# Kernel optimization log

Measured on AMD Instinct MI355X. Metric: run time of the kernel, lower is better.

The kernel has to match this reference:

```python
import jax, jax.numpy as jnp
import numpy as np

T_STEPS = 500
NHEAD = 4
L_TRANS = 2

def _pe(L, D):
    pos = np.arange(L)[:, None].astype(np.float32)
    i = np.arange(D // 2)[None, :].astype(np.float32)
    ang = pos / np.power(10000.0, 2.0 * i / D)
    pe = np.zeros((L, D), np.float32)
    pe[:, 0::2] = np.sin(ang)
    pe[:, 1::2] = np.cos(ang)
    return jnp.asarray(pe)

def _ln(x, g, b):
    m = x.mean(-1, keepdims=True)
    v = ((x - m) ** 2).mean(-1, keepdims=True)
    return (x - m) / jnp.sqrt(v + 1e-5) * g + b

def _gcn(A, X, W1, b1, W2, b2, W3, b3):
    h = jax.nn.relu((A @ X) @ W1 + b1)
    h = jax.nn.relu((A @ h) @ W2 + b2)
    return (A @ h) @ W3 + b3

def _mha(h, Wq, bq, Wk, bk, Wv, bv, Wo, bo):
    B, L, D = h.shape
    dh = D // NHEAD
    q = (h @ Wq + bq).reshape(B, L, NHEAD, dh)
    k = (h @ Wk + bk).reshape(B, L, NHEAD, dh)
    v = (h @ Wv + bv).reshape(B, L, NHEAD, dh)
    s = jnp.einsum('blhd,bmhd->bhlm', q, k) / jnp.sqrt(jnp.float32(dh))
    a = jax.nn.softmax(s, axis=-1)
    o = jnp.einsum('bhlm,bmhd->blhd', a, v).reshape(B, L, D)
    return o @ Wo + bo


def setup_inputs() -> dict:
    key = jax.random.key(0)
    ks = jax.random.split(key, 24)
    N_FP, N_WORD, DIM, HID = 10000, 4096, 20, 512
    HD1, HD2, LOUT, TDIM, FF = 128, 64, 3, 20, 2048
    N_ATOMS, N_RES, N_EDGES = 256, 4096, 65536
    w = lambda k, shp, s=0.05: jax.random.normal(k, shp, jnp.float32) * s
    idx_aa = jax.random.randint(ks[0], (N_RES,), 0, 20)
    x = jax.nn.one_hot(idx_aa, 20, dtype=jnp.float32)  # node one-hots
    adj_s = (jax.random.uniform(ks[1], (N_ATOMS, N_ATOMS)) < 0.1).astype(jnp.float32)
    return dict(
        x=x,
        smileadjacency=adj_s,
        emb_fp=w(ks[2], (N_FP, DIM)),
        emb_word=w(ks[3], (N_WORD, HID), 0.02),
        gW1=w(ks[4], (DIM, HD1)), gb1=jnp.zeros((HD1,), jnp.float32),
        gW2=w(ks[5], (HD1, HD2)), gb2=jnp.zeros((HD2,), jnp.float32),
        gW3=w(ks[6], (HD2, DIM)), gb3=jnp.zeros((DIM,), jnp.float32),
        Wq=w(ks[7], (L_TRANS, HID, HID)), bq=jnp.zeros((L_TRANS, HID), jnp.float32),
        Wk=w(ks[8], (L_TRANS, HID, HID)), bk=jnp.zeros((L_TRANS, HID), jnp.float32),
        Wv=w(ks[9], (L_TRANS, HID, HID)), bv=jnp.zeros((L_TRANS, HID), jnp.float32),
        Wo=w(ks[10], (L_TRANS, HID, HID)), bo=jnp.zeros((L_TRANS, HID), jnp.float32),
        ln1g=jnp.ones((L_TRANS, HID), jnp.float32), ln1b=jnp.zeros((L_TRANS, HID), jnp.float32),
        Wff1=w(ks[11], (L_TRANS, HID, FF)), bff1=jnp.zeros((L_TRANS, FF), jnp.float32),
        Wff2=w(ks[12], (L_TRANS, FF, HID)), bff2=jnp.zeros((L_TRANS, HID), jnp.float32),
        ln2g=jnp.ones((L_TRANS, HID), jnp.float32), ln2b=jnp.zeros((L_TRANS, HID), jnp.float32),
        Wproj=w(ks[13], (HID, DIM)), bproj=jnp.zeros((DIM,), jnp.float32),
        Wout=w(ks[14], (LOUT, 4 * DIM, 4 * DIM)), bout=jnp.zeros((LOUT, 4 * DIM), jnp.float32),
        Wtime=w(ks[15], (1, TDIM)), btime=jnp.zeros((TDIM,), jnp.float32),
        fingerprints=jax.random.randint(ks[16], (N_ATOMS,), 0, N_FP),
        words=jax.random.randint(ks[17], (N_RES,), 0, N_WORD),
        batch=jnp.zeros((N_RES,), jnp.int32),
        edge_index=jax.random.randint(ks[18], (2, N_EDGES), 0, N_RES),
        t=250,
        layer_output=3,
        dropout=0,
    )


def reference(x, smileadjacency, emb_fp, emb_word, gW1, gb1, gW2, gb2, gW3, gb3,
              Wq, bq, Wk, bk, Wv, bv, Wo, bo, ln1g, ln1b, Wff1, bff1, Wff2, bff2,
              ln2g, ln2b, Wproj, bproj, Wout, bout, Wtime, btime,
              fingerprints, words, batch, edge_index, t, layer_output, dropout):
    # --- diffusion noise (cosine alpha_bar, blosum-style transition, uniform mixing) ---
    t_float = float(t) / T_STEPS
    s = 0.008
    ab = np.cos((t_float + s) / (1 + s) * np.pi / 2) ** 2 / (np.cos(s / (1 + s) * np.pi / 2) ** 2)
    ab = jnp.float32(ab)
    Qtb = ab * jnp.eye(20, dtype=jnp.float32) + (1.0 - ab) / 20.0  # [20,20]
    prob = jnp.einsum('nij,nj->ni', Qtb[None][batch], x[:, :20])    # [n,20]
    X_t = jax.random.categorical(jax.random.key(42), jnp.log(prob + 1e-9))
    X = jax.nn.one_hot(X_t, 20, dtype=jnp.float32)
    time_emb = jnp.array([[t_float]], jnp.float32) @ Wtime + btime  # [1,20]
    # --- substrate GCN ---
    fp_vec = emb_fp[fingerprints]                                   # [n_atoms, dim]
    sub = _gcn(smileadjacency, fp_vec, gW1, gb1, gW2, gb2, gW3, gb3).mean(0, keepdims=True)
    # --- sequence transformer ---
    h = emb_word[words][None] + _pe(words.shape[0], emb_word.shape[1])[None]  # [1,L,hid]
    for l in range(L_TRANS):
        a = _mha(h, Wq[l], bq[l], Wk[l], bk[l], Wv[l], bv[l], Wo[l], bo[l])
        h = _ln(h + a, ln1g[l], ln1b[l])
        ff = jax.nn.relu(h @ Wff1[l] + bff1[l]) @ Wff2[l] + bff2[l]
        h = _ln(h + ff, ln2g[l], ln2b[l])
    seq = (h[0] @ Wproj + bproj).mean(0, keepdims=True)             # [1,dim]
    # --- protein graph: vectorized adjacency scatter (replaces per-edge python loop) ---
    n = X.shape[0]
    adj = jnp.zeros((n, n), jnp.float32).at[edge_index[0], edge_index[1]].set(1.0)
    prot = _gcn(adj, X, gW1, gb1, gW2, gb2, gW3, gb3).mean(0, keepdims=True)
    # --- fusion head (dropout=0 / eval mode) ---
    cat = jnp.concatenate([sub, prot, seq, time_emb], axis=1)        # [1, 4*dim]
    for j in range(int(layer_output)):
        cat = jax.nn.relu(cat) @ Wout[j] + bout[j]
    cat = jax.nn.relu(cat)
    return (cat, seq)
```

## Files before the change

### kernel.cpp

```cpp
#include <hip/hip_runtime.h>
#include <math.h>

typedef unsigned short ushort_t;
typedef __attribute__((ext_vector_type(8))) short bf16x8;
typedef __attribute__((ext_vector_type(4))) float f32x4;

__device__ inline float bf2f(unsigned u) { return __uint_as_float((u & 0xffffu) << 16); }
__device__ inline ushort_t f2bf(float f) {
    unsigned u = __float_as_uint(f);
    return (ushort_t)((u + 0x7fffu + ((u >> 16) & 1u)) >> 16);
}
__device__ inline void stv(float* p, float v) { *p = v; }
__device__ inline void stv(ushort_t* p, float v) { *p = f2bf(v); }
__device__ inline int guard_int(int raw, int lo, int hi) {
    if (raw >= lo && raw <= hi) return raw;
    float f = __int_as_float(raw);
    int v = (int)f;
    return (v >= lo && v <= hi) ? v : lo;
}

__device__ inline void tf2x32(unsigned k0, unsigned k1, unsigned x0, unsigned x1,
                              unsigned& o0, unsigned& o1) {
    unsigned ks2 = k0 ^ k1 ^ 0x1BD11BDAu;
    x0 += k0; x1 += k1;
#define TFR(r) { x0 += x1; x1 = (x1 << (r)) | (x1 >> (32 - (r))); x1 ^= x0; }
    TFR(13) TFR(15) TFR(26) TFR(6)  x0 += k1;  x1 += ks2 + 1u;
    TFR(17) TFR(29) TFR(16) TFR(24) x0 += ks2; x1 += k0 + 2u;
    TFR(13) TFR(15) TFR(26) TFR(6)  x0 += k0;  x1 += k1 + 3u;
    TFR(17) TFR(29) TFR(16) TFR(24) x0 += k1;  x1 += ks2 + 4u;
    TFR(13) TFR(15) TFR(26) TFR(6)  x0 += ks2; x1 += k0 + 5u;
#undef TFR
    o0 = x0; o1 = x1;
}

__global__ void k_sentinel(float* __restrict__ out, float val, int n) {
    int i = blockIdx.x * 128 + threadIdx.x;
    if (i < n) out[i] = val;
}

__global__ __launch_bounds__(256) void k_sample(const float* __restrict__ x,
                                                const int* __restrict__ t_ptr,
                                                float* __restrict__ X) {
    int i = blockIdx.x * 256 + threadIdx.x;
    if (i >= 4096) return;
    int tval = guard_int(t_ptr[0], 0, 500);
    double tf = (double)tval / 500.0;
    const double sc = 0.008;
    const double PI_HALF = 1.5707963267948966;
    double num = cos((tf + sc) / (1.0 + sc) * PI_HALF);
    double den = cos(sc / (1.0 + sc) * PI_HALF);
    float ab = (float)((num * num) / (den * den));
    float phi = (1.0f - ab) / 20.0f;
    float xv[20]; float sx = 0.f;
    for (int j = 0; j < 20; ++j) { xv[j] = x[i * 20 + j]; sx += xv[j]; }
    float best = -1e30f; int bj = 0;
    for (int j = 0; j < 20; ++j) {
        float prob = fmaxf(ab * xv[j] + phi * sx, 0.0f);
        float lp = logf(prob + 1e-9f);
        unsigned m = (unsigned)(i * 20 + j);
        unsigned o0, o1;
        tf2x32(0u, 42u, 0u, m, o0, o1);
        unsigned bits = o0 ^ o1;
        float u = __uint_as_float((bits >> 9) | 0x3f800000u) - 1.0f;
        if (u < 1.1754943508222875e-38f) u = 1.1754943508222875e-38f;
        float gmb = -logf(-logf(u));
        float z = lp + gmb;
        if (z > best) { best = z; bj = j; }
    }
    for (int j = 0; j < 20; ++j) X[i * 20 + j] = (j == bj) ? 1.0f : 0.0f;
}

__global__ __launch_bounds__(256) void k_gather_fp(const float* __restrict__ emb,
                                                   const int* __restrict__ idx,
                                                   float* __restrict__ out) {
    int i = blockIdx.x * 256 + threadIdx.x;
    if (i >= 256 * 20) return;
    int a = i / 20, d = i % 20;
    out[i] = emb[(size_t)idx[a] * 20 + d];
}

__global__ __launch_bounds__(256) void k_scatter_bits(const int* __restrict__ ei,
                                                      unsigned* __restrict__ bits) {
    int e = blockIdx.x * 256 + threadIdx.x;
    if (e >= 65536) return;
    int r = ei[e], c = ei[65536 + e];
    atomicOr(&bits[(size_t)r * 128 + (c >> 5)], 1u << (c & 31));
}

__global__ __launch_bounds__(256) void k_degree(const unsigned* __restrict__ BITS,
                                                float* __restrict__ deg) {
    int i = blockIdx.x * 256 + threadIdx.x;
    if (i >= 4096 * 128) return;
    unsigned bits = BITS[i];
    int base = (i & 127) * 32;
    while (bits) { int b = __ffs(bits) - 1; bits &= bits - 1; atomicAdd(&deg[base + b], 1.0f); }
}

__global__ __launch_bounds__(256) void k_embed(const float* __restrict__ embw,
                                               const int* __restrict__ words,
                                               float* __restrict__ H,
                                               ushort_t* __restrict__ Hb) {
    int idx = blockIdx.x * 256 + threadIdx.x;
    if (idx >= 4096 * 512) return;
    int pos = idx >> 9, d = idx & 511;
    float e = embw[(size_t)words[pos] * 512 + d];
    float expo = (float)(d >> 1) * (1.0f / 256.0f);
    float ang = (float)pos * exp2f(-expo * 13.287712379549449f);
    float pe = (d & 1) ? cosf(ang) : sinf(ang);
    float v = e + pe;
    H[idx] = v; Hb[idx] = f2bf(v);
}

__global__ __launch_bounds__(256) void k_colmean(const float* __restrict__ M, int R, int C,
                                                 float* __restrict__ out) {
    __shared__ float red[256];
    int c = blockIdx.x, t = threadIdx.x;
    float s = 0.f;
    for (int r = t; r < R; r += 256) s += M[(size_t)r * C + c];
    red[t] = s; __syncthreads();
    for (int o = 128; o; o >>= 1) { if (t < o) red[t] += red[t + o]; __syncthreads(); }
    if (t == 0) out[c] = red[0] / (float)R;
}

__global__ __launch_bounds__(256) void k_wcolsum(const float* __restrict__ M, int R, int C,
                                                 const float* __restrict__ w,
                                                 float* __restrict__ out) {
    __shared__ float red[256];
    int c = blockIdx.x, t = threadIdx.x;
    float s = 0.f;
    for (int r = t; r < R; r += 256) s += w[r] * M[(size_t)r * C + c];
    red[t] = s; __syncthreads();
    for (int o = 128; o; o >>= 1) { if (t < o) red[t] += red[t + o]; __syncthreads(); }
    if (t == 0) out[c] = red[0];
}

__global__ __launch_bounds__(256) void k_matvec20(int D, float scale,
                                                  const float* __restrict__ vec,
                                                  const float* __restrict__ W,
                                                  const float* __restrict__ bias,
                                                  float* __restrict__ out) {
    __shared__ float red[256];
    int c = blockIdx.x, t = threadIdx.x;
    float s = 0.f;
    for (int d = t; d < D; d += 256) s += vec[d] * W[(size_t)d * 20 + c];
    red[t] = s; __syncthreads();
    for (int o = 128; o; o >>= 1) { if (t < o) red[t] += red[t + o]; __syncthreads(); }
    if (t == 0) out[c] = red[0] * scale + bias[c];
}

__global__ void k_gather3(const float* __restrict__ a, const float* __restrict__ b,
                          const float* __restrict__ c, float* __restrict__ out) {
    int i = blockIdx.x * 256 + threadIdx.x;
    if (i >= 1536) return;
    out[i] = (i < 512) ? a[i] : (i < 1024) ? b[i - 512] : c[i - 1024];
}

__global__ __launch_bounds__(256) void k_castT(const float* __restrict__ in,
                                               ushort_t* __restrict__ out,
                                               int Kd, int Nd) {
    __shared__ float t[32][33];
    int bx = blockIdx.x * 32, by = blockIdx.y * 32;
    int tx = threadIdx.x & 31, ty = threadIdx.x >> 5;
#pragma unroll
    for (int i = 0; i < 4; ++i)
        t[ty + i * 8][tx] = in[(size_t)(by + ty + i * 8) * Nd + bx + tx];
    __syncthreads();
#pragma unroll
    for (int i = 0; i < 4; ++i)
        out[(size_t)(bx + ty + i * 8) * Kd + by + tx] = f2bf(t[tx][ty + i * 8]);
}

__global__ __launch_bounds__(256) void k_castT4(const float* __restrict__ in0,
                                                const float* __restrict__ in1,
                                                const float* __restrict__ in2,
                                                const float* __restrict__ in3,
                                                ushort_t* __restrict__ out) {
    __shared__ float t[32][33];
    int z = blockIdx.z;
    const float* in = (z == 0) ? in0 : (z == 1) ? in1 : (z == 2) ? in2 : in3;
    ushort_t* o = out + (size_t)z * 262144;
    int bx = blockIdx.x * 32, by = blockIdx.y * 32;
    int tx = threadIdx.x & 31, ty = threadIdx.x >> 5;
#pragma unroll
    for (int i = 0; i < 4; ++i)
        t[ty + i * 8][tx] = in[(size_t)(by + ty + i * 8) * 512 + bx + tx];
    __syncthreads();
#pragma unroll
    for (int i = 0; i < 4; ++i)
        o[(size_t)(bx + ty + i * 8) * 512 + by + tx] = f2bf(t[tx][ty + i * 8]);
}

__global__ __launch_bounds__(256) void k_transposeV(const ushort_t* __restrict__ in, int ldin,
                                                    ushort_t* __restrict__ out) {
    __shared__ ushort_t t[32][33];
    int bx = blockIdx.x * 32;
    int by = blockIdx.y * 32;
    int tx = threadIdx.x & 31, ty = threadIdx.x >> 5;
#pragma unroll
    for (int i = 0; i < 4; ++i)
        t[ty + i * 8][tx] = in[(size_t)(by + ty + i * 8) * ldin + bx + tx];
    __syncthreads();
#pragma unroll
    for (int i = 0; i < 4; ++i)
        out[(size_t)(bx + ty + i * 8) * 4096 + by + tx] = t[tx][ty + i * 8];
}

template<int BN, bool RELU, typename TC>
__global__ __launch_bounds__(256) void k_gemm_mfma2(int M, int N, int K, int lda,
        const ushort_t* __restrict__ A,
        const ushort_t* __restrict__ Bt,
        TC* __restrict__ C, int ldc,
        const float* __restrict__ bias) {
    constexpr int NJ = BN / 32;
    __shared__ ushort_t As[128][40];
    __shared__ ushort_t Bs[BN][40];
    int tid = threadIdx.x;
    int lane = tid & 63, wave = tid >> 6;
    int wr = wave >> 1, wc = wave & 1;
    int lrow = lane & 15, lq = lane >> 4;
    int br = blockIdx.y * 128, bc = blockIdx.x * BN;
    f32x4 acc[4][NJ];
#pragma unroll
    for (int i = 0; i < 4; ++i)
#pragma unroll
        for (int j = 0; j < NJ; ++j) { acc[i][j][0] = 0.f; acc[i][j][1] = 0.f; acc[i][j][2] = 0.f; acc[i][j][3] = 0.f; }
    int sr = tid >> 2, sseg = tid & 3;
    for (int k0 = 0; k0 < K; k0 += 32) {
#pragma unroll
        for (int it = 0; it < 2; ++it)
            *(uint4*)&As[sr + it * 64][sseg * 8] = *(const uint4*)&A[(size_t)(br + sr + it * 64) * lda + k0 + sseg * 8];
#pragma unroll
        for (int it = 0; it < BN / 64; ++it)
            *(uint4*)&Bs[sr + it * 64][sseg * 8] = *(const uint4*)&Bt[(size_t)(bc + sr + it * 64) * K + k0 + sseg * 8];
        __syncthreads();
        bf16x8 af[4], bfr[NJ];
#pragma unroll
        for (int i = 0; i < 4; ++i) af[i] = *(const bf16x8*)&As[wr * 64 + i * 16 + lrow][lq * 8];
#pragma unroll
        for (int j = 0; j < NJ; ++j) bfr[j] = *(const bf16x8*)&Bs[wc * (BN / 2) + j * 16 + lrow][lq * 8];
#pragma unroll
        for (int i = 0; i < 4; ++i)
#pragma unroll
            for (int j = 0; j < NJ; ++j)
                acc[i][j] = __builtin_amdgcn_mfma_f32_16x16x32_bf16(af[i], bfr[j], acc[i][j], 0, 0, 0);
        __syncthreads();
    }
#pragma unroll
    for (int i = 0; i < 4; ++i)
#pragma unroll
        for (int j = 0; j < NJ; ++j) {
            int col = bc + wc * (BN / 2) + j * 16 + lrow;
            float bv = bias ? bias[col] : 0.f;
#pragma unroll
            for (int r = 0; r < 4; ++r) {
                int row = br + wr * 64 + i * 16 + lq * 4 + r;
                float v = acc[i][j][r] + bv;
                if (RELU) v = fmaxf(v, 0.f);
                stv(&C[(size_t)row * ldc + col], v);
            }
        }
}

template<bool RELU>
__global__ __launch_bounds__(256) void k_gemm_nn(int M, int N, int K,
        const float* __restrict__ A, int lda,
        const float* __restrict__ B, int ldb,
        float* __restrict__ C, int ldc,
        const float* __restrict__ bias) {
    __shared__ float As[16][65];
    __shared__ float Bs[16][65];
    int tid = threadIdx.x;
    int tx = tid & 15, ty = tid >> 4;
    int br = blockIdx.y * 64, bc = blockIdx.x * 64;
    float acc[4][4] = {};
    for (int k0 = 0; k0 < K; k0 += 16) {
#pragma unroll
        for (int c0 = 0; c0 < 4; ++c0) {
            int r = (tid >> 4) + c0 * 16, kk = tid & 15;
            int gr = br + r, gk = k0 + kk;
            As[kk][r] = (gr < M && gk < K) ? A[(size_t)gr * lda + gk] : 0.f;
        }
#pragma unroll
        for (int c0 = 0; c0 < 4; ++c0) {
            int col = tid & 63, kk = (tid >> 6) + c0 * 4;
            int gc = bc + col, gk = k0 + kk;
            Bs[kk][col] = (gc < N && gk < K) ? B[(size_t)gk * ldb + gc] : 0.f;
        }
        __syncthreads();
#pragma unroll
        for (int kk = 0; kk < 16; ++kk) {
            float av[4], bv[4];
#pragma unroll
            for (int i2 = 0; i2 < 4; ++i2) av[i2] = As[kk][ty + 16 * i2];
#pragma unroll
            for (int j2 = 0; j2 < 4; ++j2) bv[j2] = Bs[kk][tx + 16 * j2];
#pragma unroll
            for (int i2 = 0; i2 < 4; ++i2)
#pragma unroll
                for (int j2 = 0; j2 < 4; ++j2) acc[i2][j2] += av[i2] * bv[j2];
        }
        __syncthreads();
    }
#pragma unroll
    for (int i2 = 0; i2 < 4; ++i2)
#pragma unroll
        for (int j2 = 0; j2 < 4; ++j2) {
            int r = br + ty + 16 * i2, c = bc + tx + 16 * j2;
            if (r < M && c < N) {
                float v = acc[i2][j2];
                if (bias) v += bias[c];
                if (RELU) v = fmaxf(v, 0.f);
                C[(size_t)r * ldc + c] = v;
            }
        }
}

template<int NC, int CH>
__global__ __launch_bounds__(256) void k_spmm_wave(
        const unsigned* __restrict__ BITS,
        const float* __restrict__ B, int ldb,
        float* __restrict__ C, int ldc) {
    int gw = blockIdx.x * 4 + (threadIdx.x >> 6);
    int lane = threadIdx.x & 63;
    int row = gw / CH, cb = (gw % CH) * NC;
    if (row >= 4096) return;
    float acc[NC];
#pragma unroll
    for (int j = 0; j < NC; ++j) acc[j] = 0.f;
    const unsigned* bw = &BITS[(size_t)row * 128];
#pragma unroll
    for (int i = 0; i < 2; ++i) {
        int wd = lane * 2 + i;
        unsigned bits = bw[wd];
        int base = wd * 32;
        while (bits) {
            int b = __ffs(bits) - 1; bits &= bits - 1;
            const float* br = &B[(size_t)(base + b) * ldb + cb];
#pragma unroll
            for (int j = 0; j < NC; ++j) acc[j] += br[j];
        }
    }
#pragma unroll
    for (int j = 0; j < NC; ++j) {
#pragma unroll
        for (int off = 1; off < 64; off <<= 1) acc[j] += __shfl_xor(acc[j], off, 64);
    }
    if (lane == 0)
#pragma unroll
        for (int j = 0; j < NC; ++j) C[(size_t)row * ldc + cb + j] = acc[j];
}

__global__ __launch_bounds__(256) void k_flash(const ushort_t* __restrict__ Qg, int ldq,
                                               const ushort_t* __restrict__ Kg, int ldk,
                                               const ushort_t* __restrict__ VTg,
                                               ushort_t* __restrict__ OP0,
                                               ushort_t* __restrict__ OP12,
                                               float* __restrict__ Mp,
                                               float* __restrict__ Lp) {
    __shared__ ushort_t Ks[32][136];
    __shared__ ushort_t Vt[128][40];
    __shared__ ushort_t Ps[4][16][40];
    __shared__ float    as_[4][16];
    __shared__ float    ls_[4][16];
    const int tid = threadIdx.x;
    const int lane = tid & 63, wid = tid >> 6;
    const int lrow = lane & 15, lq = lane >> 4;
    const int qb = blockIdx.x * 64, hh = blockIdx.y, z = blockIdx.z;
    const int kt0 = z * 43, kt1 = (z == 2) ? 128 : kt0 + 43;
    const float scale = 0.08838834764831845f;
    bf16x8 qf[4];
    {
        const ushort_t* qrow = &Qg[(size_t)(qb + wid * 16 + lrow) * ldq + hh * 128 + lq * 8];
#pragma unroll
        for (int s = 0; s < 4; ++s) qf[s] = *(const bf16x8*)&qrow[s * 32];
    }
    f32x4 o[8];
#pragma unroll
    for (int ct = 0; ct < 8; ++ct) { o[ct][0] = 0.f; o[ct][1] = 0.f; o[ct][2] = 0.f; o[ct][3] = 0.f; }
    float m = -INFINITY, l = 0.f;
    for (int kt = kt0; kt < kt1; ++kt) {
#pragma unroll
        for (int i = 0; i < 2; ++i) {
            int sid = tid + i * 256;
            int r = sid >> 4, sg = sid & 15;
            *(uint4*)&Ks[r][sg * 8] = *(const uint4*)&Kg[(size_t)(kt * 32 + r) * ldk + hh * 128 + sg * 8];
            int d = sid >> 2, c8 = sid & 3;
            *(uint4*)&Vt[d][c8 * 8] = *(const uint4*)&VTg[(size_t)(hh * 128 + d) * 4096 + kt * 32 + c8 * 8];
        }
        __syncthreads();
        f32x4 sa[2];
#pragma unroll
        for (int c = 0; c < 2; ++c) { sa[c][0] = 0.f; sa[c][1] = 0.f; sa[c][2] = 0.f; sa[c][3] = 0.f; }
#pragma unroll
        for (int c = 0; c < 2; ++c)
#pragma unroll
            for (int st = 0; st < 4; ++st) {
                bf16x8 kf = *(const bf16x8*)&Ks[c * 16 + lrow][st * 32 + lq * 8];
                sa[c] = __builtin_amdgcn_mfma_f32_16x16x32_bf16(kf, qf[st], sa[c], 0, 0, 0);
            }
        float s[8];
        float tm = -INFINITY;
#pragma unroll
        for (int c = 0; c < 2; ++c)
#pragma unroll
            for (int r = 0; r < 4; ++r) { float v = sa[c][r] * scale; s[c * 4 + r] = v; tm = fmaxf(tm, v); }
        tm = fmaxf(tm, __shfl_xor(tm, 16));
        tm = fmaxf(tm, __shfl_xor(tm, 32));
        bool up = tm > m;
        float mn = up ? tm : m;
        float a = up ? __expf(m - mn) : 1.0f;
        float su = 0.f;
        float p[8];
#pragma unroll
        for (int i = 0; i < 8; ++i) { p[i] = __expf(s[i] - mn); su += p[i]; }
        su += __shfl_xor(su, 16);
        su += __shfl_xor(su, 32);
        m = mn; l = l * a + su;
#pragma unroll
        for (int c = 0; c < 2; ++c)
#pragma unroll
            for (int r = 0; r < 4; ++r)
                Ps[wid][lrow][c * 16 + lq * 4 + r] = f2bf(p[c * 4 + r]);
        if (__any(up)) {
            if (lq == 0) as_[wid][lrow] = a;
            __builtin_amdgcn_s_waitcnt(0);
            float av[4];
#pragma unroll
            for (int r = 0; r < 4; ++r) av[r] = as_[wid][lq * 4 + r];
#pragma unroll
            for (int ct = 0; ct < 8; ++ct)
#pragma unroll
                for (int r = 0; r < 4; ++r) o[ct][r] *= av[r];
        } else {
            __builtin_amdgcn_s_waitcnt(0);
        }
        bf16x8 pf = *(const bf16x8*)&Ps[wid][lrow][lq * 8];
#pragma unroll
        for (int ct = 0; ct < 8; ++ct) {
            bf16x8 vf = *(const bf16x8*)&Vt[ct * 16 + lrow][lq * 8];
            o[ct] = __builtin_amdgcn_mfma_f32_16x16x32_bf16(pf, vf, o[ct], 0, 0, 0);
        }
        __syncthreads();
    }
    if (lq == 0) {
        Mp[(size_t)(z * 4 + hh) * 4096 + qb + wid * 16 + lrow] = m;
        Lp[(size_t)(z * 4 + hh) * 4096 + qb + wid * 16 + lrow] = l;
    }
    ushort_t* ob = (z == 0) ? OP0 : OP12 + (size_t)(z - 1) * 2097152;
#pragma unroll
    for (int ct = 0; ct < 8; ++ct)
#pragma unroll
        for (int r = 0; r < 4; ++r)
            ob[(size_t)(qb + wid * 16 + lq * 4 + r) * 512 + hh * 128 + ct * 16 + lrow] = f2bf(o[ct][r]);
}

__global__ __launch_bounds__(256) void k_fcomb(ushort_t* __restrict__ OP0,
                                               const ushort_t* __restrict__ OP12,
                                               const float* __restrict__ Mp,
                                               const float* __restrict__ Lp) {
    int idx = blockIdx.x * 256 + threadIdx.x;
    if (idx >= 4096 * 512) return;
    int row = idx >> 9, col = idx & 511;
    int hh = col >> 7;
    float m0 = Mp[hh * 4096 + row], m1 = Mp[(4 + hh) * 4096 + row], m2 = Mp[(8 + hh) * 4096 + row];
    float l0 = Lp[hh * 4096 + row], l1 = Lp[(4 + hh) * 4096 + row], l2 = Lp[(8 + hh) * 4096 + row];
    float mm = fmaxf(m0, fmaxf(m1, m2));
    float w0 = __expf(m0 - mm), w1 = __expf(m1 - mm), w2 = __expf(m2 - mm);
    float denom = l0 * w0 + l1 * w1 + l2 * w2;
    float o0 = bf2f(OP0[idx]), o1 = bf2f(OP12[idx]), o2 = bf2f(OP12[2097152 + idx]);
    OP0[idx] = f2bf((o0 * w0 + o1 * w1 + o2 * w2) / denom);
}

__global__ __launch_bounds__(256) void k_add_ln(const float* __restrict__ A,
                                                const float* __restrict__ B,
                                                float* __restrict__ O,
                                                ushort_t* __restrict__ Ob,
                                                const float* __restrict__ g,
                                                const float* __restrict__ b) {
    __shared__ float xr[512];
    __shared__ float red[256];
    int row = blockIdx.x, t = threadIdx.x;
    const float* a = A + (size_t)row * 512;
    const float* bb = B + (size_t)row * 512;
    float ls = 0.f;
    for (int j = t; j < 512; j += 256) { float v = a[j] + bb[j]; xr[j] = v; ls += v; }
    red[t] = ls; __syncthreads();
    for (int o = 128; o; o >>= 1) { if (t < o) red[t] += red[t + o]; __syncthreads(); }
    float mean = red[0] / 512.0f; __syncthreads();
    float lv = 0.f;
    for (int j = t; j < 512; j += 256) { float d = xr[j] - mean; lv += d * d; }
    red[t] = lv; __syncthreads();
    for (int o = 128; o; o >>= 1) { if (t < o) red[t] += red[t + o]; __syncthreads(); }
    float inv = 1.0f / sqrtf(red[0] / 512.0f + 1e-5f);
    float* o_ = O + (size_t)row * 512;
    ushort_t* ob = Ob + (size_t)row * 512;
    for (int j = t; j < 512; j += 256) {
        float v = (xr[j] - mean) * inv * g[j] + b[j];
        o_[j] = v; ob[j] = f2bf(v);
    }
}

__global__ __launch_bounds__(128) void k_fusion(const float* __restrict__ subv,
                                                const float* __restrict__ protv,
                                                const float* __restrict__ seqv,
                                                const float* __restrict__ Wtime,
                                                const float* __restrict__ btime,
                                                const float* __restrict__ Wout,
                                                const float* __restrict__ bout,
                                                const int* __restrict__ t_ptr,
                                                const int* __restrict__ lo_ptr,
                                                float* __restrict__ out) {
    __shared__ float cat[80];
    int t = threadIdx.x;
    int tval = guard_int(t_ptr[0], 0, 500);
    int L    = guard_int(lo_ptr[0], 0, 3);
    float tf = (float)((double)tval / 500.0);
    if (t < 20) {
        cat[t] = subv[t];
        cat[20 + t] = protv[t];
        cat[40 + t] = seqv[t];
        cat[60 + t] = tf * Wtime[t] + btime[t];
    }
    __syncthreads();
    for (int j = 0; j < L; ++j) {
        float acc = 0.f;
        if (t < 80) {
            for (int i2 = 0; i2 < 80; ++i2)
                acc += fmaxf(cat[i2], 0.f) * Wout[(size_t)j * 6400 + i2 * 80 + t];
            acc += bout[j * 80 + t];
        }
        __syncthreads();
        if (t < 80) cat[t] = acc;
        __syncthreads();
    }
    if (t < 80) out[t] = fmaxf(cat[t], 0.f);
    if (t < 20) out[80 + t] = seqv[t];
}

extern "C" void kernel_launch(void* const* d_in, const int* in_sizes, int n_in,
                              void* d_out, int out_size, void* d_ws, size_t ws_size,
                              hipStream_t stream) {
    static const int EXP[39] = {
        81920, 65536, 200000, 2097152, 2560, 128, 8192, 64, 1280, 20,
        524288, 1024, 524288, 1024, 524288, 1024, 524288, 1024, 1024, 1024,
        2097152, 4096, 2097152, 1024, 1024, 1024, 10240, 20, 19200, 240,
        20, 20, 256, 4096, 4096, 131072, 1, 1, 1 };
    float code = 0.f;
    if (n_in != 39) code = 900.f;
    else {
        for (int i = 0; i < 39; ++i)
            if (in_sizes[i] != EXP[i]) { code = 500.f + 4.f * (float)i; break; }
    }
    const size_t REQ = (size_t)46 * 1024 * 1024;
    if (code == 0.f && ws_size < REQ) code = (float)(ws_size >> 20);
    float* out = (float*)d_out;
    if (code != 0.f) {
        k_sentinel<<<1, 128, 0, stream>>>(out, -code, out_size);
        return;
    }

    const float* x_in   = (const float*)d_in[0];
    const float* adjs_in= (const float*)d_in[1];
    const float* embfp  = (const float*)d_in[2];
    const float* embw   = (const float*)d_in[3];
    const float* gW1 = (const float*)d_in[4];  const float* gb1 = (const float*)d_in[5];
    const float* gW2 = (const float*)d_in[6];  const float* gb2 = (const float*)d_in[7];
    const float* gW3 = (const float*)d_in[8];  const float* gb3 = (const float*)d_in[9];
    const float* Wq  = (const float*)d_in[10]; const float* bq  = (const float*)d_in[11];
    const float* Wk  = (const float*)d_in[12]; const float* bk  = (const float*)d_in[13];
    const float* Wv  = (const float*)d_in[14]; const float* bv  = (const float*)d_in[15];
    const float* Wo  = (const float*)d_in[16]; const float* bo  = (const float*)d_in[17];
    const float* ln1g= (const float*)d_in[18]; const float* ln1b= (const float*)d_in[19];
    const float* Wff1= (const float*)d_in[20]; const float* bff1= (const float*)d_in[21];
    const float* Wff2= (const float*)d_in[22]; const float* bff2= (const float*)d_in[23];
    const float* ln2g= (const float*)d_in[24]; const float* ln2b= (const float*)d_in[25];
    const float* Wproj=(const float*)d_in[26]; const float* bproj=(const float*)d_in[27];
    const float* Woutw=(const float*)d_in[28]; const float* boutw=(const float*)d_in[29];
    const float* Wtime=(const float*)d_in[30]; const float* btime=(const float*)d_in[31];
    const int* fingerprints = (const int*)d_in[32];
    const int* words        = (const int*)d_in[33];
    const int* edge_index   = (const int*)d_in[35];
    const int* t_ptr        = (const int*)d_in[36];
    const int* lo_ptr       = (const int*)d_in[37];

    char* wsb = (char*)d_ws;
    float*    misc = (float*)wsb;
    float*    H    = (float*)(wsb + ((size_t)2  << 20));
    ushort_t* Hb   = (ushort_t*)(wsb + ((size_t)10 << 20));
    ushort_t* QKVb = (ushort_t*)(wsb + ((size_t)14 << 20));
    ushort_t* Ob   = (ushort_t*)(wsb + ((size_t)26 << 20));
    ushort_t* FFHb = (ushort_t*)(wsb + ((size_t)14 << 20));
    float*    T    = (float*)(wsb + ((size_t)30 << 20));
    ushort_t* OP12 = (ushort_t*)(wsb + ((size_t)30 << 20));
    ushort_t* Wscr = (ushort_t*)(wsb + ((size_t)38 << 20));
    ushort_t* VTg  = (ushort_t*)(wsb + ((size_t)42 << 20));
    unsigned* ADJB = (unsigned*)(wsb + ((size_t)26 << 20));
    float* pt0  = (float*)(wsb + ((size_t)14 << 20));
    float* ph1  = pt0 + 81920;
    float* pt1  = ph1 + 524288;
    float* ph2  = pt1 + 524288;
    float* Xoh  = misc;
    float* fpv  = misc + 81920;
    float* st0  = misc + 87040;
    float* sh1  = misc + 92160;
    float* st1  = misc + 124928;
    float* sh2  = misc + 157696;
    float* st2  = misc + 174080;
    float* sgo  = misc + 190464;
    float* subv = misc + 277504;
    float* protv= misc + 277536;
    float* seqv = misc + 277568;
    float* hmean= misc + 280000;
    float* wsum = misc + 281000;
    float* deg  = misc + 282000;
    float* bqkv = misc + 287000;
    float* Mp   = misc + 300000;
    float* Lp   = misc + 360000;

    auto g2 = [](int M, int N) { return dim3((unsigned)((N + 63) / 64), (unsigned)((M + 63) / 64), 1); };
    auto gm64  = [](int M, int N) { return dim3((unsigned)(N / 64), (unsigned)(M / 128), 1); };
    auto gm128 = [](int M, int N) { return dim3((unsigned)(N / 128), (unsigned)(M / 128), 1); };
    auto gt = [](int Kd, int Nd) { return dim3((unsigned)(Nd / 32), (unsigned)(Kd / 32), 1); };

    k_sample<<<16, 256, 0, stream>>>(x_in, t_ptr, Xoh);

    k_gather_fp<<<20, 256, 0, stream>>>(embfp, fingerprints, fpv);
    k_gemm_nn<false><<<g2(256, 20), 256, 0, stream>>>(256, 20, 256, adjs_in, 256, fpv, 20, st0, 20, nullptr);
    k_gemm_nn<true ><<<g2(256, 128), 256, 0, stream>>>(256, 128, 20, st0, 20, gW1, 128, sh1, 128, gb1);
    k_gemm_nn<false><<<g2(256, 128), 256, 0, stream>>>(256, 128, 256, adjs_in, 256, sh1, 128, st1, 128, nullptr);
    k_gemm_nn<true ><<<g2(256, 64), 256, 0, stream>>>(256, 64, 128, st1, 128, gW2, 64, sh2, 64, gb2);
    k_gemm_nn<false><<<g2(256, 64), 256, 0, stream>>>(256, 64, 256, adjs_in, 256, sh2, 64, st2, 64, nullptr);
    k_gemm_nn<false><<<g2(256, 20), 256, 0, stream>>>(256, 20, 64, st2, 64, gW3, 20, sgo, 20, gb3);
    k_colmean<<<20, 256, 0, stream>>>(sgo, 256, 20, subv);

    k_embed<<<8192, 256, 0, stream>>>(embw, words, H, Hb);
    for (int l = 0; l < 2; ++l) {
        k_castT4<<<dim3(16, 16, 4), 256, 0, stream>>>(Wq + (size_t)l * 262144, Wk + (size_t)l * 262144,
                                                      Wv + (size_t)l * 262144, Wo + (size_t)l * 262144, Wscr);
        k_gather3<<<6, 256, 0, stream>>>(bq + l * 512, bk + l * 512, bv + l * 512, bqkv);
        k_gemm_mfma2<64, false, ushort_t><<<gm64(4096, 1536), 256, 0, stream>>>(4096, 1536, 512, 512, Hb, Wscr, QKVb, 1536, bqkv);
        k_transposeV<<<dim3(16, 128, 1), 256, 0, stream>>>(QKVb + 1024, 1536, VTg);
        k_flash<<<dim3(64, 4, 3), 256, 0, stream>>>(QKVb, 1536, QKVb + 512, 1536, VTg, Ob, OP12, Mp, Lp);
        k_fcomb<<<8192, 256, 0, stream>>>(Ob, OP12, Mp, Lp);
        k_gemm_mfma2<64, false, float><<<gm64(4096, 512), 256, 0, stream>>>(4096, 512, 512, 512, Ob, Wscr + 786432, T, 512, bo + l * 512);
        k_add_ln<<<4096, 256, 0, stream>>>(H, T, H, Hb, ln1g + l * 512, ln1b + l * 512);
        k_castT<<<gt(512, 2048), 256, 0, stream>>>(Wff1 + (size_t)l * 1048576, Wscr, 512, 2048);
        k_gemm_mfma2<128, true, ushort_t><<<gm128(4096, 2048), 256, 0, stream>>>(4096, 2048, 512, 512, Hb, Wscr, FFHb, 2048, bff1 + l * 2048);
        k_castT<<<gt(2048, 512), 256, 0, stream>>>(Wff2 + (size_t)l * 1048576, Wscr, 2048, 512);
        k_gemm_mfma2<64, false, float><<<gm64(4096, 512), 256, 0, stream>>>(4096, 512, 2048, 2048, FFHb, Wscr, T, 512, bff2 + l * 512);
        k_add_ln<<<4096, 256, 0, stream>>>(H, T, H, Hb, ln2g + l * 512, ln2b + l * 512);
    }

    k_colmean<<<512, 256, 0, stream>>>(H, 4096, 512, hmean);
    k_matvec20<<<20, 256, 0, stream>>>(512, 1.0f, hmean, Wproj, bproj, seqv);

    hipMemsetAsync(ADJB, 0, (size_t)4096 * 128 * 4, stream);
    hipMemsetAsync(deg, 0, 4096 * 4, stream);
    k_scatter_bits<<<256, 256, 0, stream>>>(edge_index, ADJB);
    k_spmm_wave<20, 1><<<1024, 256, 0, stream>>>(ADJB, Xoh, 20, pt0, 20);
    k_gemm_nn<true ><<<g2(4096, 128), 256, 0, stream>>>(4096, 128, 20, pt0, 20, gW1, 128, ph1, 128, gb1);
    k_spmm_wave<32, 4><<<4096, 256, 0, stream>>>(ADJB, ph1, 128, pt1, 128);
    k_gemm_nn<true ><<<g2(4096, 64), 256, 0, stream>>>(4096, 64, 128, pt1, 128, gW2, 64, ph2, 64, gb2);
    k_degree<<<2048, 256, 0, stream>>>(ADJB, deg);
    k_wcolsum<<<64, 256, 0, stream>>>(ph2, 4096, 64, deg, wsum);
    k_matvec20<<<20, 256, 0, stream>>>(64, 1.0f / 4096.0f, wsum, gW3, gb3, protv);

    k_fusion<<<1, 128, 0, stream>>>(subv, protv, seqv, Wtime, btime, Woutw, boutw, t_ptr, lo_ptr, out);
}
```

Before: 870.0 us.

## Fuse V transpose into QKV GEMM epilogue, simplify small GEMMs, pack P stores

The QKV GEMM epilogue now writes the V columns directly in transposed layout as packed bf16 pairs, which removes the separate k_transposeV kernel and its extra pass over V. The small GCN GEMMs switch from a shared-memory tiled kernel to a simpler 16-row-tile kernel with no LDS staging, which launches more blocks on these tiny problems. In flash attention, the bf16 probability tile is written to LDS as packed 64-bit stores. The transposed V stores are strided 8-byte writes, and the simpler GEMM reads A without coalescing.

```diff
diff --git a/kernel.cpp b/kernel.cpp
--- a/kernel.cpp
+++ b/kernel.cpp
@@ -9,6 +9,9 @@
 __device__ inline ushort_t f2bf(float f) {
     unsigned u = __float_as_uint(f);
     return (ushort_t)((u + 0x7fffu + ((u >> 16) & 1u)) >> 16);
+}
+__device__ inline unsigned pack2(float a, float b) {
+    return (unsigned)f2bf(a) | ((unsigned)f2bf(b) << 16);
 }
 __device__ inline void stv(float* p, float v) { *p = v; }
 __device__ inline void stv(ushort_t* p, float v) { *p = f2bf(v); }
@@ -190,27 +193,13 @@
         o[(size_t)(bx + ty + i * 8) * 512 + by + tx] = f2bf(t[tx][ty + i * 8]);
 }
 
-__global__ __launch_bounds__(256) void k_transposeV(const ushort_t* __restrict__ in, int ldin,
-                                                    ushort_t* __restrict__ out) {
-    __shared__ ushort_t t[32][33];
-    int bx = blockIdx.x * 32;
-    int by = blockIdx.y * 32;
-    int tx = threadIdx.x & 31, ty = threadIdx.x >> 5;
-#pragma unroll
-    for (int i = 0; i < 4; ++i)
-        t[ty + i * 8][tx] = in[(size_t)(by + ty + i * 8) * ldin + bx + tx];
-    __syncthreads();
-#pragma unroll
-    for (int i = 0; i < 4; ++i)
-        out[(size_t)(bx + ty + i * 8) * 4096 + by + tx] = t[tx][ty + i * 8];
-}
-
-template<int BN, bool RELU, typename TC>
+template<int BN, bool RELU, bool VTR, typename TC>
 __global__ __launch_bounds__(256) void k_gemm_mfma2(int M, int N, int K, int lda,
         const ushort_t* __restrict__ A,
         const ushort_t* __restrict__ Bt,
         TC* __restrict__ C, int ldc,
-        const float* __restrict__ bias) {
+        const float* __restrict__ bias,
+        ushort_t* __restrict__ VT) {
     constexpr int NJ = BN / 32;
     __shared__ ushort_t As[128][40];
     __shared__ ushort_t Bs[BN][40];
@@ -251,68 +240,53 @@
         for (int j = 0; j < NJ; ++j) {
             int col = bc + wc * (BN / 2) + j * 16 + lrow;
             float bv = bias ? bias[col] : 0.f;
-#pragma unroll
-            for (int r = 0; r < 4; ++r) {
-                int row = br + wr * 64 + i * 16 + lq * 4 + r;
-                float v = acc[i][j][r] + bv;
-                if (RELU) v = fmaxf(v, 0.f);
-                stv(&C[(size_t)row * ldc + col], v);
+            int row0 = br + wr * 64 + i * 16 + lq * 4;
+            if (VTR && col >= 1024) {
+                uint2 w;
+                w.x = pack2(acc[i][j][0] + bv, acc[i][j][1] + bv);
+                w.y = pack2(acc[i][j][2] + bv, acc[i][j][3] + bv);
+                *(uint2*)&VT[(size_t)(col - 1024) * 4096 + row0] = w;
+            } else {
+#pragma unroll
+                for (int r = 0; r < 4; ++r) {
+                    float v = acc[i][j][r] + bv;
+                    if (RELU) v = fmaxf(v, 0.f);
+                    stv(&C[(size_t)(row0 + r) * ldc + col], v);
+                }
             }
         }
 }
 
 template<bool RELU>
-__global__ __launch_bounds__(256) void k_gemm_nn(int M, int N, int K,
+__global__ __launch_bounds__(256) void k_gemm_nn16(int M, int N, int K,
         const float* __restrict__ A, int lda,
         const float* __restrict__ B, int ldb,
         float* __restrict__ C, int ldc,
         const float* __restrict__ bias) {
-    __shared__ float As[16][65];
-    __shared__ float Bs[16][65];
-    int tid = threadIdx.x;
-    int tx = tid & 15, ty = tid >> 4;
-    int br = blockIdx.y * 64, bc = blockIdx.x * 64;
-    float acc[4][4] = {};
-    for (int k0 = 0; k0 < K; k0 += 16) {
-#pragma unroll
-        for (int c0 = 0; c0 < 4; ++c0) {
-            int r = (tid >> 4) + c0 * 16, kk = tid & 15;
-            int gr = br + r, gk = k0 + kk;
-            As[kk][r] = (gr < M && gk < K) ? A[(size_t)gr * lda + gk] : 0.f;
-        }
-#pragma unroll
-        for (int c0 = 0; c0 < 4; ++c0) {
-            int col = tid & 63, kk = (tid >> 6) + c0 * 4;
-            int gc = bc + col, gk = k0 + kk;
-            Bs[kk][col] = (gc < N && gk < K) ? B[(size_t)gk * ldb + gc] : 0.f;
-        }
-        __syncthreads();
-#pragma unroll
-        for (int kk = 0; kk < 16; ++kk) {
-            float av[4], bv[4];
-#pragma unroll
-            for (int i2 = 0; i2 < 4; ++i2) av[i2] = As[kk][ty + 16 * i2];
-#pragma unroll
-            for (int j2 = 0; j2 < 4; ++j2) bv[j2] = Bs[kk][tx + 16 * j2];
-#pragma unroll
-            for (int i2 = 0; i2 < 4; ++i2)
-#pragma unroll
-                for (int j2 = 0; j2 < 4; ++j2) acc[i2][j2] += av[i2] * bv[j2];
-        }
-        __syncthreads();
-    }
-#pragma unroll
-    for (int i2 = 0; i2 < 4; ++i2)
-#pragma unroll
-        for (int j2 = 0; j2 < 4; ++j2) {
-            int r = br + ty + 16 * i2, c = bc + tx + 16 * j2;
-            if (r < M && c < N) {
-                float v = acc[i2][j2];
-                if (bias) v += bias[c];
-                if (RELU) v = fmaxf(v, 0.f);
-                C[(size_t)r * ldc + c] = v;
-            }
-        }
+    int tx = threadIdx.x & 63, ty = threadIdx.x >> 6;
+    int br = blockIdx.y * 16, bc = blockIdx.x * 64;
+    int col = bc + tx;
+    bool cok = col < N;
+    float acc[4] = {0.f, 0.f, 0.f, 0.f};
+    for (int k = 0; k < K; ++k) {
+        float b = cok ? B[(size_t)k * ldb + col] : 0.f;
+#pragma unroll
+        for (int i = 0; i < 4; ++i) {
+            int row = br + ty * 4 + i;
+            if (row < M) acc[i] += A[(size_t)row * lda + k] * b;
+        }
+    }
+    if (!cok) return;
+    float bv = bias ? bias[col] : 0.f;
+#pragma unroll
+    for (int i = 0; i < 4; ++i) {
+        int row = br + ty * 4 + i;
+        if (row < M) {
+            float v = acc[i] + bv;
+            if (RELU) v = fmaxf(v, 0.f);
+            C[(size_t)row * ldc + col] = v;
+        }
+    }
 }
 
 template<int NC, int CH>
@@ -417,10 +391,12 @@
         su += __shfl_xor(su, 32);
         m = mn; l = l * a + su;
 #pragma unroll
-        for (int c = 0; c < 2; ++c)
-#pragma unroll
-            for (int r = 0; r < 4; ++r)
-                Ps[wid][lrow][c * 16 + lq * 4 + r] = f2bf(p[c * 4 + r]);
+        for (int c = 0; c < 2; ++c) {
+            uint2 w;
+            w.x = pack2(p[c * 4 + 0], p[c * 4 + 1]);
+            w.y = pack2(p[c * 4 + 2], p[c * 4 + 3]);
+            *(uint2*)&Ps[wid][lrow][c * 16 + lq * 4] = w;
+        }
         if (__any(up)) {
             if (lq == 0) as_[wid][lrow] = a;
             __builtin_amdgcn_s_waitcnt(0);
@@ -617,7 +593,7 @@
     float* Mp   = misc + 300000;
     float* Lp   = misc + 360000;
 
-    auto g2 = [](int M, int N) { return dim3((unsigned)((N + 63) / 64), (unsigned)((M + 63) / 64), 1); };
+    auto g16 = [](int M, int N) { return dim3((unsigned)((N + 63) / 64), (unsigned)((M + 15) / 16), 1); };
     auto gm64  = [](int M, int N) { return dim3((unsigned)(N / 64), (unsigned)(M / 128), 1); };
     auto gm128 = [](int M, int N) { return dim3((unsigned)(N / 128), (unsigned)(M / 128), 1); };
     auto gt = [](int Kd, int Nd) { return dim3((unsigned)(Nd / 32), (unsigned)(Kd / 32), 1); };
@@ -625,12 +601,12 @@
     k_sample<<<16, 256, 0, stream>>>(x_in, t_ptr, Xoh);
 
     k_gather_fp<<<20, 256, 0, stream>>>(embfp, fingerprints, fpv);
-    k_gemm_nn<false><<<g2(256, 20), 256, 0, stream>>>(256, 20, 256, adjs_in, 256, fpv, 20, st0, 20, nullptr);
-    k_gemm_nn<true ><<<g2(256, 128), 256, 0, stream>>>(256, 128, 20, st0, 20, gW1, 128, sh1, 128, gb1);
-    k_gemm_nn<false><<<g2(256, 128), 256, 0, stream>>>(256, 128, 256, adjs_in, 256, sh1, 128, st1, 128, nullptr);
-    k_gemm_nn<true ><<<g2(256, 64), 256, 0, stream>>>(256, 64, 128, st1, 128, gW2, 64, sh2, 64, gb2);
-    k_gemm_nn<false><<<g2(256, 64), 256, 0, stream>>>(256, 64, 256, adjs_in, 256, sh2, 64, st2, 64, nullptr);
-    k_gemm_nn<false><<<g2(256, 20), 256, 0, stream>>>(256, 20, 64, st2, 64, gW3, 20, sgo, 20, gb3);
+    k_gemm_nn16<false><<<g16(256, 20), 256, 0, stream>>>(256, 20, 256, adjs_in, 256, fpv, 20, st0, 20, nullptr);
+    k_gemm_nn16<true ><<<g16(256, 128), 256, 0, stream>>>(256, 128, 20, st0, 20, gW1, 128, sh1, 128, gb1);
+    k_gemm_nn16<false><<<g16(256, 128), 256, 0, stream>>>(256, 128, 256, adjs_in, 256, sh1, 128, st1, 128, nullptr);
+    k_gemm_nn16<true ><<<g16(256, 64), 256, 0, stream>>>(256, 64, 128, st1, 128, gW2, 64, sh2, 64, gb2);
+    k_gemm_nn16<false><<<g16(256, 64), 256, 0, stream>>>(256, 64, 256, adjs_in, 256, sh2, 64, st2, 64, nullptr);
+    k_gemm_nn16<false><<<g16(256, 20), 256, 0, stream>>>(256, 20, 64, st2, 64, gW3, 20, sgo, 20, gb3);
     k_colmean<<<20, 256, 0, stream>>>(sgo, 256, 20, subv);
 
     k_embed<<<8192, 256, 0, stream>>>(embw, words, H, Hb);
@@ -638,16 +614,19 @@
         k_castT4<<<dim3(16, 16, 4), 256, 0, stream>>>(Wq + (size_t)l * 262144, Wk + (size_t)l * 262144,
                                                       Wv + (size_t)l * 262144, Wo + (size_t)l * 262144, Wscr);
         k_gather3<<<6, 256, 0, stream>>>(bq + l * 512, bk + l * 512, bv + l * 512, bqkv);
-        k_gemm_mfma2<64, false, ushort_t><<<gm64(4096, 1536), 256, 0, stream>>>(4096, 1536, 512, 512, Hb, Wscr, QKVb, 1536, bqkv);
-        k_transposeV<<<dim3(16, 128, 1), 256, 0, stream>>>(QKVb + 1024, 1536, VTg);
+        k_gemm_mfma2<64, false, true, ushort_t><<<gm64(4096, 1536), 256, 0, stream>>>(
+            4096, 1536, 512, 512, Hb, Wscr, QKVb, 1536, bqkv, VTg);
         k_flash<<<dim3(64, 4, 3), 256, 0, stream>>>(QKVb, 1536, QKVb + 512, 1536, VTg, Ob, OP12, Mp, Lp);
         k_fcomb<<<8192, 256, 0, stream>>>(Ob, OP12, Mp, Lp);
-        k_gemm_mfma2<64, false, float><<<gm64(4096, 512), 256, 0, stream>>>(4096, 512, 512, 512, Ob, Wscr + 786432, T, 512, bo + l * 512);
+        k_gemm_mfma2<64, false, false, float><<<gm64(4096, 512), 256, 0, stream>>>(
+            4096, 512, 512, 512, Ob, Wscr + 786432, T, 512, bo + l * 512, nullptr);
         k_add_ln<<<4096, 256, 0, stream>>>(H, T, H, Hb, ln1g + l * 512, ln1b + l * 512);
         k_castT<<<gt(512, 2048), 256, 0, stream>>>(Wff1 + (size_t)l * 1048576, Wscr, 512, 2048);
-        k_gemm_mfma2<128, true, ushort_t><<<gm128(4096, 2048), 256, 0, stream>>>(4096, 2048, 512, 512, Hb, Wscr, FFHb, 2048, bff1 + l * 2048);
+        k_gemm_mfma2<128, true, false, ushort_t><<<gm128(4096, 2048), 256, 0, stream>>>(
+            4096, 2048, 512, 512, Hb, Wscr, FFHb, 2048, bff1 + l * 2048, nullptr);
         k_castT<<<gt(2048, 512), 256, 0, stream>>>(Wff2 + (size_t)l * 1048576, Wscr, 2048, 512);
-        k_gemm_mfma2<64, false, float><<<gm64(4096, 512), 256, 0, stream>>>(4096, 512, 2048, 2048, FFHb, Wscr, T, 512, bff2 + l * 512);
+        k_gemm_mfma2<64, false, false, float><<<gm64(4096, 512), 256, 0, stream>>>(
+            4096, 512, 2048, 2048, FFHb, Wscr, T, 512, bff2 + l * 512, nullptr);
         k_add_ln<<<4096, 256, 0, stream>>>(H, T, H, Hb, ln2g + l * 512, ln2b + l * 512);
     }
 
@@ -658,9 +637,9 @@
     hipMemsetAsync(deg, 0, 4096 * 4, stream);
     k_scatter_bits<<<256, 256, 0, stream>>>(edge_index, ADJB);
     k_spmm_wave<20, 1><<<1024, 256, 0, stream>>>(ADJB, Xoh, 20, pt0, 20);
-    k_gemm_nn<true ><<<g2(4096, 128), 256, 0, stream>>>(4096, 128, 20, pt0, 20, gW1, 128, ph1, 128, gb1);
+    k_gemm_nn16<true ><<<g16(4096, 128), 256, 0, stream>>>(4096, 128, 20, pt0, 20, gW1, 128, ph1, 128, gb1);
     k_spmm_wave<32, 4><<<4096, 256, 0, stream>>>(ADJB, ph1, 128, pt1, 128);
-    k_gemm_nn<true ><<<g2(4096, 64), 256, 0, stream>>>(4096, 64, 128, pt1, 128, gW2, 64, ph2, 64, gb2);
+    k_gemm_nn16<true ><<<g16(4096, 64), 256, 0, stream>>>(4096, 64, 128, pt1, 128, gW2, 64, ph2, 64, gb2);
     k_degree<<<2048, 256, 0, stream>>>(ADJB, deg);
     k_wcolsum<<<64, 256, 0, stream>>>(ph2, 4096, 64, deg, wsum);
     k_matvec20<<<20, 256, 0, stream>>>(64, 1.0f / 4096.0f, wsum, gW3, gb3, protv);
```

After: 1.189 ms. +36.6%, slower.
